# Performance work log

Measured on AMD Instinct MI355X. Metric: run time of the kernel, lower is better.

## Reference

```python
import jax, jax.numpy as jnp
import numpy as np

N = 100000
F_IN = 128
E = 1_600_000
NEG_SLOPE = 0.2  # PyG GATConv default negative_slope


def _seg_sum(v, idx, n):
    return jax.ops.segment_sum(v, idx, num_segments=n)


def gcn_conv(x, W, b, src, dst, n):
    # PyG GCNConv: D^{-1/2} (A + I) D^{-1/2} X W + b (self loops already in src/dst)
    h = x @ W
    deg = _seg_sum(jnp.ones(src.shape, h.dtype), dst, n)
    dinv = jnp.where(deg > 0, jax.lax.rsqrt(deg), 0.0)
    norm = dinv[src] * dinv[dst]  # [E]
    return _seg_sum(h[src] * norm[:, None], dst, n) + b


def gat_conv(x, W, a_src, a_dst, b, src, dst, n, heads, out_ch):
    # PyG GATConv (concat=True), eval mode (dropout inactive)
    h = (x @ W).reshape(n, heads, out_ch)          # [n,H,C]
    s = jnp.einsum('nhc,hc->nh', h, a_src)          # per-node src score
    t = jnp.einsum('nhc,hc->nh', h, a_dst)          # per-node dst score
    e = jax.nn.leaky_relu(s[src] + t[dst], NEG_SLOPE)  # [E,H]
    m = jax.ops.segment_max(e, dst, num_segments=n)    # stable segment softmax
    m = jnp.where(jnp.isfinite(m), m, 0.0)
    p = jnp.exp(e - m[dst])
    denom = _seg_sum(p, dst, n)
    alpha = p / (denom[dst] + 1e-16)                 # [E,H]
    out = _seg_sum(h[src] * alpha[:, :, None], dst, n)  # [n,H,C]
    return out.reshape(n, heads * out_ch) + b


def setup_inputs():
    key = jax.random.key(0)
    ks = jax.random.split(key, 24)
    x = jax.random.normal(ks[0], (N, F_IN), jnp.float32) * 0.1
    half = N // 2
    # one-hot user/item type flags read by forward (x[:,0]==1 / x[:,1]==1)
    x = x.at[:, 0].set(0.0).at[:, 1].set(0.0)
    x = x.at[:half, 0].set(1.0).at[half:, 1].set(1.0)
    src = jax.random.randint(ks[1], (E,), 0, N, dtype=jnp.int32)
    dst = jax.random.randint(ks[2], (E,), 0, N, dtype=jnp.int32)
    edge_index = jnp.stack([src, dst])

    def p(k, shape):
        return jax.random.normal(k, shape, jnp.float32) * 0.1

    inp = {"x": x, "edge_index": edge_index,
           "gcn_w": p(ks[3], (F_IN, 16)), "gcn_b": jnp.zeros((16,), jnp.float32)}
    dims = [(16, 16, 8), (128, 16, 8), (128, 16, 8), (128, 2, 1)]
    for i, (fi, fo, h) in enumerate(dims, start=1):
        inp[f"g{i}_w"] = p(ks[3 + 4 * i], (fi, h * fo))
        inp[f"g{i}_as"] = p(ks[4 + 4 * i], (h, fo))
        inp[f"g{i}_ad"] = p(ks[5 + 4 * i], (h, fo))
        inp[f"g{i}_b"] = jnp.zeros((h * fo,), jnp.float32)
    return inp


def reference(x, edge_index, gcn_w, gcn_b,
              g1_w, g1_as, g1_ad, g1_b,
              g2_w, g2_as, g2_ad, g2_b,
              g3_w, g3_as, g3_ad, g3_b,
              g4_w, g4_as, g4_ad, g4_b):
    n = x.shape[0]
    loops = jnp.arange(n, dtype=edge_index.dtype)  # self loops (added by GCN/GAT layers)
    src = jnp.concatenate([edge_index[0], loops])
    dst = jnp.concatenate([edge_index[1], loops])
    h = jax.nn.elu(gcn_conv(x, gcn_w, gcn_b, src, dst, n))
    h = jax.nn.elu(gat_conv(h, g1_w, g1_as, g1_ad, g1_b, src, dst, n, 8, 16))
    h = jax.nn.elu(gat_conv(h, g2_w, g2_as, g2_ad, g2_b, src, dst, n, 8, 16))
    h = jax.nn.elu(gat_conv(h, g3_w, g3_as, g3_ad, g3_b, src, dst, n, 8, 16))
    h = jax.nn.elu(gat_conv(h, g4_w, g4_as, g4_ad, g4_b, src, dst, n, 1, 2))  # [n,2]
    half = n // 2  # users are rows [:half], items rows [half:]
    out = jnp.concatenate([h[:half], h[half:]], axis=1)  # [half,4]
    return jax.nn.log_softmax(out, axis=1)
```

## Files before the change

### kernel.cpp

```cpp
#include <hip/hip_runtime.h>
#include <cstddef>
#include <cstdint>

#define NN 100000
#define NPAD 100032
#define NE 1600000
#define ET (NE + NN)
#define ETP_MAX (ET + 4 * NN)
#define HALFN (NN / 2)
#define NEG_SLOPE 0.2f
#define SCB 1024
#define RP 8
#define RNODES (NN / RP)
#define CHUNK 8192

typedef __attribute__((ext_vector_type(8))) short short8v;
typedef __attribute__((ext_vector_type(4))) float float4v;
typedef __attribute__((ext_vector_type(2))) float float2v;

__device__ __forceinline__ float lrelu(float x) { return x > 0.f ? x : NEG_SLOPE * x; }

__device__ __forceinline__ uint16_t f2bf(float f) {
  uint32_t u = __float_as_uint(f);
  uint32_t r = u + 0x7fffu + ((u >> 16) & 1u);
  return (uint16_t)(r >> 16);
}
__device__ __forceinline__ float bflo(uint32_t u) { return __uint_as_float(u << 16); }
__device__ __forceinline__ float bfhi(uint32_t u) { return __uint_as_float(u & 0xffff0000u); }

template<int K, int M>
__launch_bounds__(256)
__global__ void gemm4_kernel(const float* __restrict__ X, const float* __restrict__ W,
                             float* __restrict__ Y, int n) {
  constexpr int CG = M / 4;
  constexpr int RG = 256 / CG;
  constexpr int RPT = 2;
  constexpr int RT = RG * RPT;
  constexpr int KP = K + 1;
  __shared__ __align__(16) float sW[K * M];
  __shared__ float sX[RT * KP];
  for (int i = threadIdx.x; i < K * M; i += 256) sW[i] = W[i];
  const int jg = threadIdx.x % CG;
  const int rg = threadIdx.x / CG;
  const int r0 = rg * RPT;
  for (int base = blockIdx.x * RT; base < n; base += gridDim.x * RT) {
    __syncthreads();
    const int nrows = (n - base) < RT ? (n - base) : RT;
    for (int i = threadIdx.x; i < nrows * K; i += 256) {
      int r = i / K, c = i - r * K;
      sX[r * KP + c] = X[(size_t)base * K + i];
    }
    __syncthreads();
    float acc[RPT][4];
    #pragma unroll
    for (int rr = 0; rr < RPT; ++rr) acc[rr][0] = acc[rr][1] = acc[rr][2] = acc[rr][3] = 0.f;
    #pragma unroll 4
    for (int k = 0; k < K; ++k) {
      const float4 w = *(const float4*)&sW[k * M + jg * 4];
      #pragma unroll
      for (int rr = 0; rr < RPT; ++rr) {
        const float xv = sX[(r0 + rr) * KP + k];
        acc[rr][0] = fmaf(xv, w.x, acc[rr][0]);
        acc[rr][1] = fmaf(xv, w.y, acc[rr][1]);
        acc[rr][2] = fmaf(xv, w.z, acc[rr][2]);
        acc[rr][3] = fmaf(xv, w.w, acc[rr][3]);
      }
    }
    #pragma unroll
    for (int rr = 0; rr < RPT; ++rr) {
      if (r0 + rr < nrows) {
        float4 o = make_float4(acc[rr][0], acc[rr][1], acc[rr][2], acc[rr][3]);
        *(float4*)&Y[(size_t)(base + r0 + rr) * M + jg * 4] = o;
      }
    }
  }
}

template<int KB>
__launch_bounds__(256)
__global__ void wpack_kernel(const float* __restrict__ W, uint16_t* __restrict__ wp,
                             int Kreal) {
  int tid = blockIdx.x * 256 + threadIdx.x;
  if (tid >= KB * 8 * 64) return;
  int lane = tid & 63;
  int ctkb = tid >> 6;
  int kb = ctkb % KB, ct = ctkb / KB;
  int nc = ct * 16 + (lane & 15);
  int k0 = kb * 32 + (lane >> 4) * 8;
  ushort4 o0, o1;
  uint16_t v[8];
  #pragma unroll
  for (int j = 0; j < 8; ++j) {
    int k = k0 + j;
    v[j] = (k < Kreal) ? f2bf(W[(size_t)k * 128 + nc]) : (uint16_t)0;
  }
  o0.x = v[0]; o0.y = v[1]; o0.z = v[2]; o0.w = v[3];
  o1.x = v[4]; o1.y = v[5]; o1.z = v[6]; o1.w = v[7];
  *(ushort4*)&wp[(size_t)tid * 8] = o0;
  *(ushort4*)&wp[(size_t)tid * 8 + 4] = o1;
}

template<int KB, int XS>
__launch_bounds__(256)
__global__ void gemm_mfma_kernel(const uint16_t* __restrict__ X,
                                 const uint16_t* __restrict__ wp,
                                 uint16_t* __restrict__ Y, int n) {
  __shared__ float sC[4][16 * 136];
  const int wv = threadIdx.x >> 6;
  const int lane = threadIdx.x & 63;
  const int rowbase = blockIdx.x * 64 + wv * 16;
  int arow = rowbase + (lane & 15);
  if (arow >= n) arow = n - 1;
  const uint16_t* xp = X + (size_t)arow * XS + ((lane >> 4) * 8);
  short8v a[KB];
  #pragma unroll
  for (int kb = 0; kb < KB; ++kb) a[kb] = *(const short8v*)(xp + kb * 32);
  #pragma unroll
  for (int ct = 0; ct < 8; ++ct) {
    float4v acc = {0.f, 0.f, 0.f, 0.f};
    #pragma unroll
    for (int kb = 0; kb < KB; ++kb) {
      short8v b = *(const short8v*)&wp[(size_t)((ct * KB + kb) * 64 + lane) * 8];
      acc = __builtin_amdgcn_mfma_f32_16x16x32_bf16(a[kb], b, acc, 0, 0, 0);
    }
    #pragma unroll
    for (int r = 0; r < 4; ++r)
      sC[wv][((lane >> 4) * 4 + r) * 136 + ct * 16 + (lane & 15)] = acc[r];
  }
  #pragma unroll
  for (int t = 0; t < 4; ++t) {
    int idx = t * 64 + lane;
    int row = idx >> 4;
    int c8 = idx & 15;
    const float* pr = &sC[wv][row * 136 + c8 * 8];
    float4 lo = *(const float4*)pr;
    float4 hi = *(const float4*)(pr + 4);
    uint4 o;
    o.x = (uint32_t)f2bf(lo.x) | ((uint32_t)f2bf(lo.y) << 16);
    o.y = (uint32_t)f2bf(lo.z) | ((uint32_t)f2bf(lo.w) << 16);
    o.z = (uint32_t)f2bf(hi.x) | ((uint32_t)f2bf(hi.y) << 16);
    o.w = (uint32_t)f2bf(hi.z) | ((uint32_t)f2bf(hi.w) << 16);
    *(uint4*)&Y[(size_t)(rowbase + row) * 128 + c8 * 8] = o;
  }
}

template<int K, int M, int ROWS>
__launch_bounds__(256)
__global__ void gemm_s_kernel(const uint16_t* __restrict__ Xb, const float* __restrict__ W,
                              float* __restrict__ Y, int n) {
  constexpr int KP = K + 1;
  __shared__ float sW[K * M];
  __shared__ float sX[ROWS * KP];
  for (int i = threadIdx.x; i < K * M; i += 256) sW[i] = W[i];
  for (int base = blockIdx.x * ROWS; base < n; base += gridDim.x * ROWS) {
    __syncthreads();
    const int nrows = (n - base) < ROWS ? (n - base) : ROWS;
    for (int i = threadIdx.x; i < nrows * (K / 4); i += 256) {
      int r = i / (K / 4), c = i - r * (K / 4);
      uint2 u = *(const uint2*)&Xb[(size_t)(base + r) * K + c * 4];
      sX[r * KP + c * 4 + 0] = bflo(u.x);
      sX[r * KP + c * 4 + 1] = bfhi(u.x);
      sX[r * KP + c * 4 + 2] = bflo(u.y);
      sX[r * KP + c * 4 + 3] = bfhi(u.y);
    }
    __syncthreads();
    for (int o = threadIdx.x; o < nrows * M; o += 256) {
      int r = o / M, j = o - r * M;
      float a = 0.f;
      #pragma unroll
      for (int k = 0; k < K; ++k) a = fmaf(sX[r * KP + k], sW[k * M + j], a);
      Y[(size_t)(base + r) * M + j] = a;
    }
  }
}

template<int H, int C>
__launch_bounds__(256)
__global__ void score_bf16_kernel(const uint32_t* __restrict__ Hm,
                                  const float* __restrict__ aS, const float* __restrict__ aD,
                                  float* __restrict__ S, float* __restrict__ T, int n) {
  int idx = blockIdx.x * 256 + threadIdx.x;
  int tot = n * H;
  if (idx >= tot + H) return;
  if (idx >= tot) { S[idx] = -1e30f; T[idx] = 0.f; return; }
  int h = idx & (H - 1);
  const uint32_t* hp = Hm + (size_t)idx * (C / 2);
  float s = 0.f, t = 0.f;
  #pragma unroll
  for (int c2 = 0; c2 < C / 2; ++c2) {
    uint32_t u = hp[c2];
    float v0 = bflo(u), v1 = bfhi(u);
    s = fmaf(v0, aS[h * C + 2 * c2], s);
    s = fmaf(v1, aS[h * C + 2 * c2 + 1], s);
    t = fmaf(v0, aD[h * C + 2 * c2], t);
    t = fmaf(v1, aD[h * C + 2 * c2 + 1], t);
  }
  S[idx] = s;
  T[idx] = t;
}

template<int H, int C>
__launch_bounds__(256)
__global__ void score_kernel(const float* __restrict__ Hm,
                             const float* __restrict__ aS, const float* __restrict__ aD,
                             float* __restrict__ S, float* __restrict__ T, int n) {
  int idx = blockIdx.x * 256 + threadIdx.x;
  int tot = n * H;
  if (idx >= tot + H) return;
  if (idx >= tot) { S[idx] = -1e30f; T[idx] = 0.f; return; }
  int h = idx & (H - 1);
  const float* hp = Hm + (size_t)idx * C;
  float s = 0.f, t = 0.f;
  #pragma unroll
  for (int c = 0; c < C; ++c) {
    float v = hp[c];
    s = fmaf(v, aS[h * C + c], s);
    t = fmaf(v, aD[h * C + c], t);
  }
  S[idx] = s;
  T[idx] = t;
}

__launch_bounds__(256)
__global__ void rank_kernel(const int* __restrict__ edst, int* __restrict__ cursor,
                            int* __restrict__ rank) {
  int e = blockIdx.x * 256 + threadIdx.x;
  if (e >= ET) return;
  int dn = e < NE ? edst[e] : e - NE;
  rank[e] = atomicAdd(&cursor[dn], 1);
}

__device__ __forceinline__ int pad4(int d) { return (d + 3) & ~3; }

__launch_bounds__(256)
__global__ void scan1_kernel(const int* __restrict__ degi, int* __restrict__ rowptr,
                             int* __restrict__ bsums) {
  __shared__ int sd[256];
  int t = threadIdx.x;
  int base = blockIdx.x * SCB + t * 4;
  int v0 = base + 0 < NN ? pad4(degi[base + 0]) : 0;
  int v1 = base + 1 < NN ? pad4(degi[base + 1]) : 0;
  int v2 = base + 2 < NN ? pad4(degi[base + 2]) : 0;
  int v3 = base + 3 < NN ? pad4(degi[base + 3]) : 0;
  int s = v0 + v1 + v2 + v3;
  sd[t] = s;
  __syncthreads();
  for (int off = 1; off < 256; off <<= 1) {
    int x = (t >= off) ? sd[t - off] : 0;
    __syncthreads();
    sd[t] += x;
    __syncthreads();
  }
  int excl = sd[t] - s;
  if (t == 255) bsums[blockIdx.x] = sd[255];
  if (base + 0 < NN) rowptr[base + 0] = excl;
  excl += v0;
  if (base + 1 < NN) rowptr[base + 1] = excl;
  excl += v1;
  if (base + 2 < NN) rowptr[base + 2] = excl;
  excl += v2;
  if (base + 3 < NN) rowptr[base + 3] = excl;
}

__launch_bounds__(256)
__global__ void scan2_kernel(int* __restrict__ bsums, int nb) {
  __shared__ int sd[256];
  int t = threadIdx.x;
  int v = t < nb ? bsums[t] : 0;
  sd[t] = v;
  __syncthreads();
  for (int off = 1; off < 256; off <<= 1) {
    int x = (t >= off) ? sd[t - off] : 0;
    __syncthreads();
    sd[t] += x;
    __syncthreads();
  }
  if (t < nb) bsums[t] = sd[t] - v;
  if (t == nb - 1) bsums[nb] = sd[t];
}

__launch_bounds__(256)
__global__ void scan3_kernel(int* __restrict__ rowptr, const int* __restrict__ bsums, int nb) {
  int i = blockIdx.x * 256 + threadIdx.x;
  if (i < NN) rowptr[i] += bsums[i / SCB];
  if (i == 0) rowptr[NN] = bsums[nb];
}

__launch_bounds__(256)
__global__ void dinv_kernel(const int* __restrict__ deg, float* __restrict__ dinv) {
  int i = blockIdx.x * 256 + threadIdx.x;
  if (i > NN) return;
  if (i == NN) { dinv[i] = 0.f; return; }
  int d = deg[i];
  dinv[i] = d > 0 ? rsqrtf((float)d) : 0.f;
}

__launch_bounds__(256)
__global__ void csr_fill_kernel(int* __restrict__ csr) {
  int i = blockIdx.x * 256 + threadIdx.x;
  if (i < ETP_MAX) csr[i] = NN;
}

__launch_bounds__(256)
__global__ void scatter_part_kernel(const int* __restrict__ esrc, const int* __restrict__ edst,
                                    const int* __restrict__ rowptr, const int* __restrict__ rank,
                                    int* __restrict__ csr_src) {
  int p = blockIdx.x & (RP - 1);
  int c = blockIdx.x >> 3;
  int lo = p * RNODES, hi = lo + RNODES;
  int e0 = c * CHUNK;
  int e1 = e0 + CHUNK < ET ? e0 + CHUNK : ET;
  for (int e = e0 + threadIdx.x; e < e1; e += 256) {
    int dn = e < NE ? edst[e] : e - NE;
    if (dn >= lo && dn < hi) {
      int sn = e < NE ? esrc[e] : e - NE;
      csr_src[rowptr[dn] + rank[e]] = sn;
    }
  }
}

__launch_bounds__(256)
__global__ void fused_gat_kernel(const int* __restrict__ rowptr, const int* __restrict__ csr,
                                 const float* __restrict__ S, const float* __restrict__ T,
                                 const uint16_t* __restrict__ Hm, const float* __restrict__ bias,
                                 uint16_t* __restrict__ Outb) {
  const int lane = threadIdx.x & 63;
  const int d = (blockIdx.x * 256 + threadIdx.x) >> 6;
  if (d >= NN) return;
  const int rs = rowptr[d];
  const int deg = rowptr[d + 1] - rs;
  const int eg = lane >> 4;
  const int cl = lane & 15;
  const int hp = cl >> 1;
  const float Th = T[(size_t)d * 8 + hp];
  const char* sb = (const char*)S;
  const char* hb = (const char*)Hm;
  float m = -1e38f;
  float s = 0.f;
  float2v A0 = {0.f, 0.f}, A1 = {0.f, 0.f}, A2 = {0.f, 0.f}, A3 = {0.f, 0.f};
  const uint32_t clo = (uint32_t)(cl << 4);
  const uint32_t hpo = (uint32_t)(hp << 2);
  for (int l0 = 0; l0 < deg; l0 += 4) {
    int lc = l0 + eg;
    int sn = csr[rs + lc];
    uint4 u = *(const uint4*)(hb + (((uint32_t)sn << 8) + clo));
    float sv = *(const float*)(sb + (((uint32_t)sn << 5) + hpo));
    float e = lrelu(sv + Th);
    float nm = fmaxf(m, e);
    float p = __expf(e - nm);
    if (e > m) {
      float sc = __expf(m - nm);
      float2v scv = {sc, sc};
      s *= sc;
      A0 *= scv; A1 *= scv; A2 *= scv; A3 *= scv;
      m = nm;
    }
    s += p;
    float2v pp = {p, p};
    A0 = pp * (float2v){bflo(u.x), bfhi(u.x)} + A0;
    A1 = pp * (float2v){bflo(u.y), bfhi(u.y)} + A1;
    A2 = pp * (float2v){bflo(u.z), bfhi(u.z)} + A2;
    A3 = pp * (float2v){bflo(u.w), bfhi(u.w)} + A3;
  }
  #pragma unroll
  for (int mask = 16; mask <= 32; mask <<= 1) {
    float om = __shfl_xor(m, mask);
    float os = __shfl_xor(s, mask);
    float o0x = __shfl_xor(A0.x, mask), o0y = __shfl_xor(A0.y, mask);
    float o1x = __shfl_xor(A1.x, mask), o1y = __shfl_xor(A1.y, mask);
    float o2x = __shfl_xor(A2.x, mask), o2y = __shfl_xor(A2.y, mask);
    float o3x = __shfl_xor(A3.x, mask), o3y = __shfl_xor(A3.y, mask);
    float nm = fmaxf(m, om);
    float s1 = __expf(m - nm), s2 = __expf(om - nm);
    s = s * s1 + os * s2;
    A0.x = A0.x * s1 + o0x * s2; A0.y = A0.y * s1 + o0y * s2;
    A1.x = A1.x * s1 + o1x * s2; A1.y = A1.y * s1 + o1y * s2;
    A2.x = A2.x * s1 + o2x * s2; A2.y = A2.y * s1 + o2y * s2;
    A3.x = A3.x * s1 + o3x * s2; A3.y = A3.y * s1 + o3y * s2;
    m = nm;
  }
  if (lane < 16) {
    const float inv = 1.f / (s + 1e-16f);
    float4 b0 = *(const float4*)&bias[cl * 8];
    float4 b1 = *(const float4*)&bias[cl * 8 + 4];
    float v0 = fmaf(A0.x, inv, b0.x), v1 = fmaf(A0.y, inv, b0.y);
    float v2 = fmaf(A1.x, inv, b0.z), v3 = fmaf(A1.y, inv, b0.w);
    float v4 = fmaf(A2.x, inv, b1.x), v5 = fmaf(A2.y, inv, b1.y);
    float v6 = fmaf(A3.x, inv, b1.z), v7 = fmaf(A3.y, inv, b1.w);
    v0 = v0 > 0.f ? v0 : expm1f(v0); v1 = v1 > 0.f ? v1 : expm1f(v1);
    v2 = v2 > 0.f ? v2 : expm1f(v2); v3 = v3 > 0.f ? v3 : expm1f(v3);
    v4 = v4 > 0.f ? v4 : expm1f(v4); v5 = v5 > 0.f ? v5 : expm1f(v5);
    v6 = v6 > 0.f ? v6 : expm1f(v6); v7 = v7 > 0.f ? v7 : expm1f(v7);
    uint4 o;
    o.x = (uint32_t)f2bf(v0) | ((uint32_t)f2bf(v1) << 16);
    o.y = (uint32_t)f2bf(v2) | ((uint32_t)f2bf(v3) << 16);
    o.z = (uint32_t)f2bf(v4) | ((uint32_t)f2bf(v5) << 16);
    o.w = (uint32_t)f2bf(v6) | ((uint32_t)f2bf(v7) << 16);
    *(uint4*)&Outb[(size_t)d * 128 + cl * 8] = o;
  }
}

__launch_bounds__(256)
__global__ void fused_gat1_kernel(const int* __restrict__ rowptr, const int* __restrict__ csr,
                                  const float* __restrict__ S, const float* __restrict__ T,
                                  const float* __restrict__ Hm2, const float* __restrict__ bias,
                                  float* __restrict__ galpha, float* __restrict__ Out) {
  int d = (blockIdx.x * 256 + threadIdx.x) >> 6;
  if (d >= NN) return;
  int lane = threadIdx.x & 63;
  int rs = rowptr[d], deg = rowptr[d + 1] - rs;
  float Td = T[d];
  int sn = 0;
  float e = -1e30f;
  if (lane < deg) { sn = csr[rs + lane]; e = lrelu(S[sn] + Td); }
  float m = e;
  for (int l2 = 64 + lane; l2 < deg; l2 += 64) {
    float e2 = lrelu(S[csr[rs + l2]] + Td);
    galpha[rs + l2] = e2;
    m = fmaxf(m, e2);
  }
  #pragma unroll
  for (int mask = 1; mask < 64; mask <<= 1) m = fmaxf(m, __shfl_xor(m, mask));
  float p = (lane < deg) ? __expf(e - m) : 0.f;
  float sum = p;
  for (int l2 = 64 + lane; l2 < deg; l2 += 64) {
    float p2 = __expf(galpha[rs + l2] - m);
    galpha[rs + l2] = p2;
    sum += p2;
  }
  #pragma unroll
  for (int mask = 1; mask < 64; mask <<= 1) sum += __shfl_xor(sum, mask);
  float inv = 1.f / (sum + 1e-16f);
  float a0 = 0.f, a1 = 0.f;
  if (lane < deg) {
    float2 hv = *(const float2*)&Hm2[(size_t)sn * 2];
    a0 = p * hv.x; a1 = p * hv.y;
  }
  for (int l2 = 64 + lane; l2 < deg; l2 += 64) {
    int sn2 = csr[rs + l2];
    float p2 = galpha[rs + l2];
    float2 hv = *(const float2*)&Hm2[(size_t)sn2 * 2];
    a0 = fmaf(p2, hv.x, a0); a1 = fmaf(p2, hv.y, a1);
  }
  #pragma unroll
  for (int mask = 1; mask < 64; mask <<= 1) {
    a0 += __shfl_xor(a0, mask); a1 += __shfl_xor(a1, mask);
  }
  if (lane == 0) {
    float v0 = fmaf(a0, inv, bias[0]);
    float v1 = fmaf(a1, inv, bias[1]);
    v0 = v0 > 0.f ? v0 : expm1f(v0);
    v1 = v1 > 0.f ? v1 : expm1f(v1);
    float2 o; o.x = v0; o.y = v1;
    *(float2*)&Out[(size_t)d * 2] = o;
  }
}

__launch_bounds__(256)
__global__ void gcn_pull_kernel(const int* __restrict__ rowptr, const int* __restrict__ csr_src,
                                const float* __restrict__ dinv, const float* __restrict__ Hm,
                                const float* __restrict__ bias, uint16_t* __restrict__ Outb) {
  int d = blockIdx.x * 16 + threadIdx.x / 16;
  if (d >= NN) return;
  int f = threadIdx.x & 15;
  int rs = rowptr[d], re = rowptr[d + 1];
  float acc = 0.f;
  int j = rs;
  for (; j + 4 <= re; j += 4) {
    int s0 = csr_src[j], s1 = csr_src[j + 1], s2 = csr_src[j + 2], s3 = csr_src[j + 3];
    float d0 = dinv[s0], d1 = dinv[s1], d2 = dinv[s2], d3 = dinv[s3];
    float h0 = Hm[(size_t)s0 * 16 + f], h1 = Hm[(size_t)s1 * 16 + f];
    float h2 = Hm[(size_t)s2 * 16 + f], h3 = Hm[(size_t)s3 * 16 + f];
    acc = fmaf(d0, h0, acc); acc = fmaf(d1, h1, acc);
    acc = fmaf(d2, h2, acc); acc = fmaf(d3, h3, acc);
  }
  for (; j < re; ++j) {
    int sn = csr_src[j];
    acc = fmaf(dinv[sn], Hm[(size_t)sn * 16 + f], acc);
  }
  float v = acc * dinv[d] + bias[f];
  v = v > 0.f ? v : expm1f(v);
  Outb[(size_t)d * 32 + f] = f2bf(v);
  Outb[(size_t)d * 32 + 16 + f] = 0;
}

__launch_bounds__(256)
__global__ void final_kernel(const float* __restrict__ A, float* __restrict__ Out) {
  int i = blockIdx.x * 256 + threadIdx.x;
  if (i >= HALFN) return;
  float v0 = A[(size_t)i * 2 + 0];
  float v1 = A[(size_t)i * 2 + 1];
  float v2 = A[(size_t)(i + HALFN) * 2 + 0];
  float v3 = A[(size_t)(i + HALFN) * 2 + 1];
  float m = fmaxf(fmaxf(v0, v1), fmaxf(v2, v3));
  float e0 = __expf(v0 - m), e1 = __expf(v1 - m), e2 = __expf(v2 - m), e3 = __expf(v3 - m);
  float l = logf(e0 + e1 + e2 + e3) + m;
  Out[(size_t)i * 4 + 0] = v0 - l;
  Out[(size_t)i * 4 + 1] = v1 - l;
  Out[(size_t)i * 4 + 2] = v2 - l;
  Out[(size_t)i * 4 + 3] = v3 - l;
}

extern "C" void kernel_launch(void* const* d_in, const int* in_sizes, int n_in,
                              void* d_out, int out_size, void* d_ws, size_t ws_size,
                              hipStream_t stream) {
  const float* x     = (const float*)d_in[0];
  const int*   eidx  = (const int*)d_in[1];
  const int*   esrc  = eidx;
  const int*   edst  = eidx + NE;
  const float* gcn_w = (const float*)d_in[2];
  const float* gcn_b = (const float*)d_in[3];

  char* ws = (char*)d_ws;
  uint16_t* hbf    = (uint16_t*)(ws + 0);
  uint16_t* bufAb  = (uint16_t*)(ws + 25700000);
  uint16_t* gcnHbf = (uint16_t*)(ws + 51400000);
  float*    bufB   = (float*)   (ws + 57900000);
  float*    bufC   = (float*)   (ws + 64400000);
  float*    Sb     = (float*)   (ws + 65300000);
  float*    Tb     = (float*)   (ws + 68600000);
  float*    galpha = (float*)   (ws + 71900000);
  int*      rowptr = (int*)     (ws + 151900000);
  int*      cursor = (int*)     (ws + 152300008);
  int*      csr    = (int*)     (ws + 152700008);
  float*    dinv   = (float*)   (ws + 162700008);
  int*      bsums  = (int*)     (ws + 163100016);
  int*      rank   = (int*)     (ws + 163100528);
  uint16_t* wpck   = (uint16_t*)(ws + 169900528);

  constexpr int NB_SCAN = (NN + SCB - 1) / SCB;

  hipMemsetAsync(cursor, 0, (size_t)NN * 4, stream);
  rank_kernel<<<(ET + 255) / 256, 256, 0, stream>>>(edst, cursor, rank);
  scan1_kernel<<<NB_SCAN, 256, 0, stream>>>(cursor, rowptr, bsums);
  scan2_kernel<<<1, 256, 0, stream>>>(bsums, NB_SCAN);
  scan3_kernel<<<(NN + 256) / 256, 256, 0, stream>>>(rowptr, bsums, NB_SCAN);
  dinv_kernel<<<(NN + 256) / 256, 256, 0, stream>>>(cursor, dinv);
  csr_fill_kernel<<<(ETP_MAX + 255) / 256, 256, 0, stream>>>(csr);
  {
    int nch = (ET + CHUNK - 1) / CHUNK;
    scatter_part_kernel<<<nch * RP, 256, 0, stream>>>(esrc, edst, rowptr, rank, csr);
  }

  {
    int tiles = (NN + 127) / 128;
    if (tiles > 4096) tiles = 4096;
    gemm4_kernel<128, 16><<<tiles, 256, 0, stream>>>(x, gcn_w, bufB, NN);
  }
  gcn_pull_kernel<<<(NN + 15) / 16, 256, 0, stream>>>(rowptr, csr, dinv, bufB, gcn_b, gcnHbf);

  wpack_kernel<1><<<2, 256, 0, stream>>>((const float*)d_in[4], wpck, 16);
  gemm_mfma_kernel<1, 32><<<NPAD / 64, 256, 0, stream>>>(gcnHbf, wpck, hbf, NN);
  score_bf16_kernel<8, 16><<<(NN * 8 + 8 + 255) / 256, 256, 0, stream>>>(
      (const uint32_t*)hbf, (const float*)d_in[5], (const float*)d_in[6], Sb, Tb, NN);
  fused_gat_kernel<<<(NN * 64 + 255) / 256, 256, 0, stream>>>(
      rowptr, csr, Sb, Tb, hbf, (const float*)d_in[7], bufAb);

  wpack_kernel<4><<<8, 256, 0, stream>>>((const float*)d_in[8], wpck, 128);
  gemm_mfma_kernel<4, 128><<<NPAD / 64, 256, 0, stream>>>(bufAb, wpck, hbf, NN);
  score_bf16_kernel<8, 16><<<(NN * 8 + 8 + 255) / 256, 256, 0, stream>>>(
      (const uint32_t*)hbf, (const float*)d_in[9], (const float*)d_in[10], Sb, Tb, NN);
  fused_gat_kernel<<<(NN * 64 + 255) / 256, 256, 0, stream>>>(
      rowptr, csr, Sb, Tb, hbf, (const float*)d_in[11], bufAb);

  wpack_kernel<4><<<8, 256, 0, stream>>>((const float*)d_in[12], wpck, 128);
  gemm_mfma_kernel<4, 128><<<NPAD / 64, 256, 0, stream>>>(bufAb, wpck, hbf, NN);
  score_bf16_kernel<8, 16><<<(NN * 8 + 8 + 255) / 256, 256, 0, stream>>>(
      (const uint32_t*)hbf, (const float*)d_in[13], (const float*)d_in[14], Sb, Tb, NN);
  fused_gat_kernel<<<(NN * 64 + 255) / 256, 256, 0, stream>>>(
      rowptr, csr, Sb, Tb, hbf, (const float*)d_in[15], bufAb);

  {
    int tiles = (NN + 127) / 128;
    if (tiles > 2048) tiles = 2048;
    gemm_s_kernel<128, 2, 128><<<tiles, 256, 0, stream>>>(
        bufAb, (const float*)d_in[16], bufB, NN);
    score_kernel<1, 2><<<(NN + 1 + 255) / 256, 256, 0, stream>>>(
        bufB, (const float*)d_in[17], (const float*)d_in[18], Sb, Tb, NN);
    fused_gat1_kernel<<<(NN * 64 + 255) / 256, 256, 0, stream>>>(
        rowptr, csr, Sb, Tb, bufB, (const float*)d_in[19], galpha, bufC);
  }

  final_kernel<<<(HALFN + 255) / 256, 256, 0, stream>>>(bufC, (float*)d_out);
}
```

Baseline: 588.7 us.

## Fuse GAT attention scores into MFMA GEMM epilogue and unroll edge loop by two

Computes the per-node source and destination attention scores directly from the fp32 GEMM tile held in shared memory, which removes three separate score kernels and their re-read of the bf16 features. The scores now come from fp32 values rather than bf16-rounded ones. Separately, CSR rows are padded to multiples of 8 and the fused GAT aggregation processes two neighbours per lane per iteration, prefetching the next indices to raise memory-level parallelism. This costs more padded edges and more registers per lane. A tiny kernel writes the padding sentinel scores.

After: 542.9 us. 1.08x faster.

```diff
diff --git a/kernel.cpp b/kernel.cpp
--- a/kernel.cpp
+++ b/kernel.cpp
@@ -6,7 +6,7 @@
 #define NPAD 100032
 #define NE 1600000
 #define ET (NE + NN)
-#define ETP_MAX (ET + 4 * NN)
+#define ETP_MAX (ET + 8 * NN)
 #define HALFN (NN / 2)
 #define NEG_SLOPE 0.2f
 #define SCB 1024
@@ -104,7 +104,9 @@
 __launch_bounds__(256)
 __global__ void gemm_mfma_kernel(const uint16_t* __restrict__ X,
                                  const uint16_t* __restrict__ wp,
-                                 uint16_t* __restrict__ Y, int n) {
+                                 const float* __restrict__ aS, const float* __restrict__ aD,
+                                 uint16_t* __restrict__ Y,
+                                 float* __restrict__ S, float* __restrict__ T, int n) {
   __shared__ float sC[4][16 * 136];
   const int wv = threadIdx.x >> 6;
   const int lane = threadIdx.x & 63;
@@ -142,6 +144,26 @@
     o.w = (uint32_t)f2bf(hi.z) | ((uint32_t)f2bf(hi.w) << 16);
     *(uint4*)&Y[(size_t)(rowbase + row) * 128 + c8 * 8] = o;
   }
+  {
+    int r = lane & 15;
+    int hg = lane >> 4;
+    int node = rowbase + r;
+    if (node < n) {
+      #pragma unroll
+      for (int hh = 0; hh < 2; ++hh) {
+        int h = hg * 2 + hh;
+        float sv = 0.f, tv = 0.f;
+        #pragma unroll
+        for (int c = 0; c < 16; ++c) {
+          float v = sC[wv][r * 136 + h * 16 + c];
+          sv = fmaf(v, aS[h * 16 + c], sv);
+          tv = fmaf(v, aD[h * 16 + c], tv);
+        }
+        S[(size_t)node * 8 + h] = sv;
+        T[(size_t)node * 8 + h] = tv;
+      }
+    }
+  }
 }
 
 template<int K, int M, int ROWS>
@@ -174,29 +196,11 @@
   }
 }
 
-template<int H, int C>
-__launch_bounds__(256)
-__global__ void score_bf16_kernel(const uint32_t* __restrict__ Hm,
-                                  const float* __restrict__ aS, const float* __restrict__ aD,
-                                  float* __restrict__ S, float* __restrict__ T, int n) {
-  int idx = blockIdx.x * 256 + threadIdx.x;
-  int tot = n * H;
-  if (idx >= tot + H) return;
-  if (idx >= tot) { S[idx] = -1e30f; T[idx] = 0.f; return; }
-  int h = idx & (H - 1);
-  const uint32_t* hp = Hm + (size_t)idx * (C / 2);
-  float s = 0.f, t = 0.f;
-  #pragma unroll
-  for (int c2 = 0; c2 < C / 2; ++c2) {
-    uint32_t u = hp[c2];
-    float v0 = bflo(u), v1 = bfhi(u);
-    s = fmaf(v0, aS[h * C + 2 * c2], s);
-    s = fmaf(v1, aS[h * C + 2 * c2 + 1], s);
-    t = fmaf(v0, aD[h * C + 2 * c2], t);
-    t = fmaf(v1, aD[h * C + 2 * c2 + 1], t);
-  }
-  S[idx] = s;
-  T[idx] = t;
+__global__ void spad_kernel(float* __restrict__ S, float* __restrict__ T) {
+  if (threadIdx.x < 8) {
+    S[(size_t)NN * 8 + threadIdx.x] = -1e30f;
+    T[(size_t)NN * 8 + threadIdx.x] = 0.f;
+  }
 }
 
 template<int H, int C>
@@ -230,7 +234,7 @@
   rank[e] = atomicAdd(&cursor[dn], 1);
 }
 
-__device__ __forceinline__ int pad4(int d) { return (d + 3) & ~3; }
+__device__ __forceinline__ int pad8(int d) { return (d + 7) & ~7; }
 
 __launch_bounds__(256)
 __global__ void scan1_kernel(const int* __restrict__ degi, int* __restrict__ rowptr,
@@ -238,10 +242,10 @@
   __shared__ int sd[256];
   int t = threadIdx.x;
   int base = blockIdx.x * SCB + t * 4;
-  int v0 = base + 0 < NN ? pad4(degi[base + 0]) : 0;
-  int v1 = base + 1 < NN ? pad4(degi[base + 1]) : 0;
-  int v2 = base + 2 < NN ? pad4(degi[base + 2]) : 0;
-  int v3 = base + 3 < NN ? pad4(degi[base + 3]) : 0;
+  int v0 = base + 0 < NN ? pad8(degi[base + 0]) : 0;
+  int v1 = base + 1 < NN ? pad8(degi[base + 1]) : 0;
+  int v2 = base + 2 < NN ? pad8(degi[base + 2]) : 0;
+  int v3 = base + 3 < NN ? pad8(degi[base + 3]) : 0;
   int s = v0 + v1 + v2 + v3;
   sd[t] = s;
   __syncthreads();
@@ -340,27 +344,40 @@
   float2v A0 = {0.f, 0.f}, A1 = {0.f, 0.f}, A2 = {0.f, 0.f}, A3 = {0.f, 0.f};
   const uint32_t clo = (uint32_t)(cl << 4);
   const uint32_t hpo = (uint32_t)(hp << 2);
-  for (int l0 = 0; l0 < deg; l0 += 4) {
-    int lc = l0 + eg;
-    int sn = csr[rs + lc];
-    uint4 u = *(const uint4*)(hb + (((uint32_t)sn << 8) + clo));
-    float sv = *(const float*)(sb + (((uint32_t)sn << 5) + hpo));
-    float e = lrelu(sv + Th);
-    float nm = fmaxf(m, e);
-    float p = __expf(e - nm);
-    if (e > m) {
+  int iA = rs + eg;
+  int snA = csr[iA];
+  int snB = csr[iA + 4];
+  for (int l0 = 0; l0 < deg; l0 += 8) {
+    int snA2 = csr[iA + 8];
+    int snB2 = csr[iA + 12];
+    uint4 uA = *(const uint4*)(hb + (((uint32_t)snA << 8) + clo));
+    uint4 uB = *(const uint4*)(hb + (((uint32_t)snB << 8) + clo));
+    float svA = *(const float*)(sb + (((uint32_t)snA << 5) + hpo));
+    float svB = *(const float*)(sb + (((uint32_t)snB << 5) + hpo));
+    iA += 8;
+    float eA = lrelu(svA + Th);
+    float eB = lrelu(svB + Th);
+    float nm = fmaxf(m, fmaxf(eA, eB));
+    if (nm > m) {
       float sc = __expf(m - nm);
       float2v scv = {sc, sc};
       s *= sc;
       A0 *= scv; A1 *= scv; A2 *= scv; A3 *= scv;
       m = nm;
     }
-    s += p;
-    float2v pp = {p, p};
-    A0 = pp * (float2v){bflo(u.x), bfhi(u.x)} + A0;
-    A1 = pp * (float2v){bflo(u.y), bfhi(u.y)} + A1;
-    A2 = pp * (float2v){bflo(u.z), bfhi(u.z)} + A2;
-    A3 = pp * (float2v){bflo(u.w), bfhi(u.w)} + A3;
+    float pA = __expf(eA - m);
+    float pB = __expf(eB - m);
+    s += pA + pB;
+    float2v ppA = {pA, pA}, ppB = {pB, pB};
+    A0 = ppA * (float2v){bflo(uA.x), bfhi(uA.x)} + A0;
+    A1 = ppA * (float2v){bflo(uA.y), bfhi(uA.y)} + A1;
+    A2 = ppA * (float2v){bflo(uA.z), bfhi(uA.z)} + A2;
+    A3 = ppA * (float2v){bflo(uA.w), bfhi(uA.w)} + A3;
+    A0 = ppB * (float2v){bflo(uB.x), bfhi(uB.x)} + A0;
+    A1 = ppB * (float2v){bflo(uB.y), bfhi(uB.y)} + A1;
+    A2 = ppB * (float2v){bflo(uB.z), bfhi(uB.z)} + A2;
+    A3 = ppB * (float2v){bflo(uB.w), bfhi(uB.w)} + A3;
+    snA = snA2; snB = snB2;
   }
   #pragma unroll
   for (int mask = 16; mask <= 32; mask <<= 1) {
@@ -541,6 +558,7 @@
     int nch = (ET + CHUNK - 1) / CHUNK;
     scatter_part_kernel<<<nch * RP, 256, 0, stream>>>(esrc, edst, rowptr, rank, csr);
   }
+  spad_kernel<<<1, 64, 0, stream>>>(Sb, Tb);
 
   {
     int tiles = (NN + 127) / 128;
@@ -550,23 +568,20 @@
   gcn_pull_kernel<<<(NN + 15) / 16, 256, 0, stream>>>(rowptr, csr, dinv, bufB, gcn_b, gcnHbf);
 
   wpack_kernel<1><<<2, 256, 0, stream>>>((const float*)d_in[4], wpck, 16);
-  gemm_mfma_kernel<1, 32><<<NPAD / 64, 256, 0, stream>>>(gcnHbf, wpck, hbf, NN);
-  score_bf16_kernel<8, 16><<<(NN * 8 + 8 + 255) / 256, 256, 0, stream>>>(
-      (const uint32_t*)hbf, (const float*)d_in[5], (const float*)d_in[6], Sb, Tb, NN);
+  gemm_mfma_kernel<1, 32><<<NPAD / 64, 256, 0, stream>>>(
+      gcnHbf, wpck, (const float*)d_in[5], (const float*)d_in[6], hbf, Sb, Tb, NN);
   fused_gat_kernel<<<(NN * 64 + 255) / 256, 256, 0, stream>>>(
       rowptr, csr, Sb, Tb, hbf, (const float*)d_in[7], bufAb);
 
   wpack_kernel<4><<<8, 256, 0, stream>>>((const float*)d_in[8], wpck, 128);
-  gemm_mfma_kernel<4, 128><<<NPAD / 64, 256, 0, stream>>>(bufAb, wpck, hbf, NN);
-  score_bf16_kernel<8, 16><<<(NN * 8 + 8 + 255) / 256, 256, 0, stream>>>(
-      (const uint32_t*)hbf, (const float*)d_in[9], (const float*)d_in[10], Sb, Tb, NN);
+  gemm_mfma_kernel<4, 128><<<NPAD / 64, 256, 0, stream>>>(
+      bufAb, wpck, (const float*)d_in[9], (const float*)d_in[10], hbf, Sb, Tb, NN);
   fused_gat_kernel<<<(NN * 64 + 255) / 256, 256, 0, stream>>>(
       rowptr, csr, Sb, Tb, hbf, (const float*)d_in[11], bufAb);
 
   wpack_kernel<4><<<8, 256, 0, stream>>>((const float*)d_in[12], wpck, 128);
-  gemm_mfma_kernel<4, 128><<<NPAD / 64, 256, 0, stream>>>(bufAb, wpck, hbf, NN);
-  score_bf16_kernel<8, 16><<<(NN * 8 + 8 + 255) / 256, 256, 0, stream>>>(
-      (const uint32_t*)hbf, (const float*)d_in[13], (const float*)d_in[14], Sb, Tb, NN);
+  gemm_mfma_kernel<4, 128><<<NPAD / 64, 256, 0, stream>>>(
+      bufAb, wpck, (const float*)d_in[13], (const float*)d_in[14], hbf, Sb, Tb, NN);
   fused_gat_kernel<<<(NN * 64 + 255) / 256, 256, 0, stream>>>(
       rowptr, csr, Sb, Tb, hbf, (const float*)d_in[15], bufAb);
 
```
